# Kernel tuning notes

Measured on AMD Instinct MI355X. Metric: run time of the kernel, lower is better.

Reference implementation:

```python
import jax, jax.numpy as jnp
import numpy as np

HEAD_DIM = 128
N_HEADS = 16
N_KV_HEADS = 4
N_REP = N_HEADS // N_KV_HEADS


def _rope(x, cos, sin):
    # x: [B, S, Hk, D]; cos/sin: [S, D/2]
    xr = x.reshape(*x.shape[:-1], -1, 2)
    x0, x1 = xr[..., 0], xr[..., 1]
    c = cos[None, :, None, :]
    s = sin[None, :, None, :]
    o0 = x0 * c - x1 * s
    o1 = x0 * s + x1 * c
    return jnp.stack([o0, o1], axis=-1).reshape(x.shape)


def setup_inputs() -> dict:
    key = jax.random.key(0)
    ks = jax.random.split(key, 7)
    B, S, DIM = 2, 1024, 2048
    KV_DIM = HEAD_DIM * N_KV_HEADS
    x = jax.random.normal(ks[0], (B, S, DIM), dtype=jnp.float32)
    # rotary angles like LLaMA: freqs = 1/10000^(2i/D)
    inv_freq = 1.0 / (10000.0 ** (np.arange(0, HEAD_DIM, 2, dtype=np.float32) / HEAD_DIM))
    ang = np.arange(S, dtype=np.float32)[:, None] * inv_freq[None, :]  # [S, D/2]
    theta_cos = jnp.asarray(np.cos(ang))
    theta_sin = jnp.asarray(np.sin(ang))
    sc = 0.02
    wq = jax.random.normal(ks[1], (DIM, DIM), dtype=jnp.float32) * sc
    wk = jax.random.normal(ks[2], (DIM, KV_DIM), dtype=jnp.float32) * sc
    wv = jax.random.normal(ks[3], (DIM, KV_DIM), dtype=jnp.float32) * sc
    wo = jax.random.normal(ks[4], (DIM, DIM), dtype=jnp.float32) * sc
    return {"x": x, "theta_cos": theta_cos, "theta_sin": theta_sin,
            "wq": wq, "wk": wk, "wv": wv, "wo": wo}


def reference(x, theta_cos, theta_sin, wq, wk, wv, wo):
    B, S, DIM = x.shape
    # projections
    xq = (x @ wq).reshape(B, S, N_HEADS, HEAD_DIM).transpose(0, 2, 1, 3)  # [B,H,S,D]
    xk = (x @ wk).reshape(B, S, N_KV_HEADS, HEAD_DIM)                      # [B,S,Hk,D]
    xv = (x @ wv).reshape(B, S, N_KV_HEADS, HEAD_DIM)
    # RoPE on K and V only (faithful to source: Q is NOT rotated)
    xk = _rope(xk, theta_cos, theta_sin)
    xv = _rope(xv, theta_cos, theta_sin)
    # GQA repeat: [B,S,Hk,D] -> [B,H,S,D] (each kv head repeated consecutively)
    xk = jnp.repeat(xk.transpose(0, 2, 1, 3), N_REP, axis=1)
    xv = jnp.repeat(xv.transpose(0, 2, 1, 3), N_REP, axis=1)
    scale = HEAD_DIM ** (-0.5)
    att = jnp.einsum('bhqd,bhkd->bhqk', xq, xk) * scale
    # faithful masking: tril then masked_fill(att == 0, -inf)
    tri = jnp.tril(jnp.ones((S, S), dtype=bool))
    att = jnp.where(tri[None, None], att, 0.0)
    att = jnp.where(att == 0.0, -jnp.inf, att)
    att = jax.nn.softmax(att, axis=-1)
    y = jnp.einsum('bhqk,bhkd->bhqd', att, xv)
    out = y.transpose(0, 2, 1, 3).reshape(B, S, DIM)
    return out @ wo
```

## Files before the change

kernel.cpp:

```cpp
#include <hip/hip_runtime.h>
#include <hip/hip_bf16.h>
#include <stdint.h>

typedef _Float16 half_t;
typedef __attribute__((ext_vector_type(2))) _Float16 h2_t;
typedef __attribute__((ext_vector_type(4))) _Float16 h4_t;
typedef __attribute__((ext_vector_type(8))) _Float16 h8_t;
typedef __attribute__((ext_vector_type(4))) float f32x4;

__device__ __forceinline__ void gload16(const void* g, void* l) {
    __builtin_amdgcn_global_load_lds(
        (const __attribute__((address_space(1))) uint32_t*)(uintptr_t)g,
        (__attribute__((address_space(3))) uint32_t*)(uint32_t)(uintptr_t)l,
        16, 0, 0);
}

__global__ __launch_bounds__(256) void prep(const float* __restrict__ x, half_t* __restrict__ xh,
                                            const float* __restrict__ wq, const float* __restrict__ wk,
                                            const float* __restrict__ wv, const float* __restrict__ wo,
                                            half_t* __restrict__ qt, half_t* __restrict__ kt,
                                            half_t* __restrict__ vt, half_t* __restrict__ ot) {
    __shared__ half_t T[32][36];
    const int bx = blockIdx.x;
    if (bx < 2048) {
        int g = (bx * 256 + threadIdx.x) * 8;
        float4 a = *(const float4*)(x + g);
        float4 b = *(const float4*)(x + g + 4);
        h8_t o = {(half_t)a.x,(half_t)a.y,(half_t)a.z,(half_t)a.w,
                  (half_t)b.x,(half_t)b.y,(half_t)b.z,(half_t)b.w};
        *(h8_t*)(xh + g) = o;
        return;
    }
    const int wb = bx - 2048;
    const float* src; half_t* dst; int Nd, t;
    if (wb < 4096)      { src = wq; dst = qt; Nd = 2048; t = wb; }
    else if (wb < 5120) { src = wk; dst = kt; Nd = 512;  t = wb - 4096; }
    else if (wb < 6144) { src = wv; dst = vt; Nd = 512;  t = wb - 5120; }
    else                { src = wo; dst = ot; Nd = 2048; t = wb - 6144; }
    const int K = 2048;
    int nt = Nd >> 5;
    int ti = t / nt, tj = t % nt;
    int r  = threadIdx.x >> 3;
    int c4 = (threadIdx.x & 7) << 2;
    float4 v = *(const float4*)(src + (size_t)(ti*32 + r) * Nd + tj*32 + c4);
    T[r][c4+0] = (half_t)v.x; T[r][c4+1] = (half_t)v.y;
    T[r][c4+2] = (half_t)v.z; T[r][c4+3] = (half_t)v.w;
    __syncthreads();
    h4_t o = {T[c4+0][r], T[c4+1][r], T[c4+2][r], T[c4+3][r]};
    *(h4_t*)(dst + (size_t)(tj*32 + r) * K + ti*32 + c4) = o;
}

template<int BM, int QKV, typename CT>
__global__ __launch_bounds__(256) void gemm_t(const half_t* __restrict__ A,
                                              const half_t* __restrict__ Bq,
                                              const half_t* __restrict__ Bk,
                                              const half_t* __restrict__ Bv,
                                              CT* __restrict__ Cq,
                                              half_t* __restrict__ Ck,
                                              half_t* __restrict__ Cv,
                                              int NB, int K) {
    constexpr int MI  = BM / 32;
    constexpr int ACH = BM / 8;
    constexpr int TOT = ACH + 16;
    constexpr int PW  = TOT / 4;
    __shared__ half_t Ah[BM * 64];
    __shared__ half_t Bh[128 * 64];
    const int tid = threadIdx.x, lane = tid & 63, wid = tid >> 6;
    const int lr = lane & 15, lg = lane >> 4;
    const int wm = wid >> 1, wn = wid & 1;
    const int nwg = gridDim.x, bid = blockIdx.x;
    const int swz = (bid & 7) * (nwg >> 3) + (bid >> 3);
    const int bm = swz / NB, bn = swz % NB;
    const int m0 = bm * BM;

    const half_t* W; CT* Cc; int cs, col0;
    if constexpr (QKV) {
        if (bn < 16)      { W = Bq + (size_t)bn * 128 * K;        Cc = Cq;       cs = 2048; col0 = bn * 128; }
        else if (bn < 20) { W = Bk + (size_t)(bn - 16) * 128 * K; Cc = (CT*)Ck;  cs = 512;  col0 = (bn - 16) * 128; }
        else              { W = Bv + (size_t)(bn - 20) * 128 * K; Cc = (CT*)Cv;  cs = 512;  col0 = (bn - 20) * 128; }
    } else {
        W = Bq + (size_t)bn * 128 * K; Cc = Cq; cs = NB * 128; col0 = bn * 128;
    }

    const half_t* Arow = A + (size_t)m0 * K;
    f32x4 acc[MI][4] = {};

    for (int k0 = 0; k0 < K; k0 += 64) {
        #pragma unroll
        for (int c = 0; c < PW; c++) {
            const int chunk = wid * PW + c;
            const int o = lane * 16;
            if (chunk < ACH) {
                const int go   = (chunk << 10) + o;
                const int row  = go >> 7;
                const int colb = (go & 127) ^ ((row & 7) << 4);
                gload16(Arow + (size_t)row * K + k0 + (colb >> 1), (char*)Ah + (chunk << 10));
            } else {
                const int go   = ((chunk - ACH) << 10) + o;
                const int row  = go >> 7;
                const int colb = (go & 127) ^ ((row & 7) << 4);
                gload16(W + (size_t)row * K + k0 + (colb >> 1), (char*)Bh + ((chunk - ACH) << 10));
            }
        }
        __syncthreads();
        h8_t af[2][MI], bf[2][4];
        #pragma unroll
        for (int kk = 0; kk < 2; kk++) {
            #pragma unroll
            for (int mi = 0; mi < MI; mi++) {
                const int row = wm * (BM / 2) + mi * 16 + lr;
                const int cb  = (kk * 64 + lg * 16) ^ ((lr & 7) << 4);
                af[kk][mi] = *(const h8_t*)((const char*)Ah + row * 128 + cb);
            }
            #pragma unroll
            for (int ni = 0; ni < 4; ni++) {
                const int row = wn * 64 + ni * 16 + lr;
                const int cb  = (kk * 64 + lg * 16) ^ ((lr & 7) << 4);
                bf[kk][ni] = *(const h8_t*)((const char*)Bh + row * 128 + cb);
            }
        }
        #pragma unroll
        for (int kk = 0; kk < 2; kk++)
            #pragma unroll
            for (int mi = 0; mi < MI; mi++)
                #pragma unroll
                for (int ni = 0; ni < 4; ni++)
                    acc[mi][ni] = __builtin_amdgcn_mfma_f32_16x16x32_f16(af[kk][mi], bf[kk][ni], acc[mi][ni], 0, 0, 0);
        __syncthreads();
    }

    #pragma unroll
    for (int mi = 0; mi < MI; mi++)
        #pragma unroll
        for (int ni = 0; ni < 4; ni++)
            #pragma unroll
            for (int r = 0; r < 4; r++) {
                int row = m0 + wm * (BM / 2) + mi * 16 + lg * 4 + r;
                int col = col0 + wn * 64 + ni * 16 + lr;
                Cc[(size_t)row * cs + col] = (CT)acc[mi][ni][r];
            }
}

__global__ __launch_bounds__(256) void rope(half_t* __restrict__ Kh, const half_t* __restrict__ Vh,
                                            half_t* __restrict__ Vt, const float* __restrict__ cs,
                                            const float* __restrict__ sn) {
    const int bx = blockIdx.x;
    if (bx < 2048) {
        int gid = bx * 256 + threadIdx.x;
        int row = gid >> 8;
        int pc  = gid & 255;
        int s   = row & 1023;
        int p   = pc & 63;
        float c = cs[s * 64 + p], si = sn[s * 64 + p];
        h2_t v = *(h2_t*)(Kh + (size_t)row * 512 + 2 * pc);
        float x0 = (float)v[0], x1 = (float)v[1];
        h2_t o = {(half_t)(x0 * c - x1 * si), (half_t)(x0 * si + x1 * c)};
        *(h2_t*)(Kh + (size_t)row * 512 + 2 * pc) = o;
        return;
    }
    int gid = (bx - 2048) * 256 + threadIdx.x;
    int col = gid & 2047;
    int dp  = gid >> 11;
    int s   = col & 1023;
    int p   = dp & 63;
    float c = cs[s * 64 + p], si = sn[s * 64 + p];
    h2_t v = *(const h2_t*)(Vh + (size_t)col * 512 + 2 * dp);
    float x0 = (float)v[0], x1 = (float)v[1];
    Vt[(size_t)(2 * dp)     * 2048 + col] = (half_t)(x0 * c - x1 * si);
    Vt[(size_t)(2 * dp + 1) * 2048 + col] = (half_t)(x0 * si + x1 * c);
}

__global__ __launch_bounds__(256) void attn4(const half_t* __restrict__ Qh, const half_t* __restrict__ Kh,
                                             const half_t* __restrict__ Vtg, half_t* __restrict__ Yh) {
    __shared__ half_t K0[64 * 128], K1[64 * 128];
    __shared__ half_t V0[128 * 64], V1[128 * 64];
    __shared__ half_t Pl[4][16][72];

    const int tid = threadIdx.x, lane = tid & 63, wid = tid >> 6;
    const int lr = lane & 15, lg = lane >> 4;
    const int bx = blockIdx.x;
    const int g  = bx & 7;
    const int local = bx >> 3;
    const int b = g >> 2, kvh = g & 3;
    const int h = kvh * 4 + (local & 3);
    const int li = local >> 2;
    const int qt = (li < 8) ? (15 - li) : (li - 8);
    const int nkb = qt + 1;
    const int qbase = qt * 64 + wid * 16;
    const size_t qrow0 = (size_t)(b * 1024 + qbase);
    const size_t kbase = (size_t)b * 1024;

    const float sc = 0.08838834764831845f;
    h8_t qf[4];
    #pragma unroll
    for (int kk = 0; kk < 4; kk++) {
        qf[kk] = *(const h8_t*)(Qh + (qrow0 + lr) * 2048 + h * 128 + kk * 32 + lg * 8);
        qf[kk] = qf[kk] * (half_t)sc;
    }

    float m[4], l[4];
    f32x4 yacc[8] = {};
    #pragma unroll
    for (int r = 0; r < 4; r++) { m[r] = -1e30f; l[r] = 0.f; }

    auto stage = [&](half_t* kt, half_t* vb, int kb) {
        const int j = kb * 64;
        #pragma unroll
        for (int c = 0; c < 4; c++) {
            const int chunk = wid * 4 + c;
            const int o = (chunk << 10) + lane * 16;
            { const int row  = o >> 8;
              const int colb = (o & 255) ^ ((row & 7) << 4);
              gload16(Kh + (kbase + j + row) * 512 + kvh * 128 + (colb >> 1),
                      (char*)kt + (chunk << 10)); }
            { const int row  = o >> 7;
              const int colb = (o & 127) ^ ((row & 7) << 4);
              gload16(Vtg + (size_t)(kvh * 128 + row) * 2048 + kbase + j + (colb >> 1),
                      (char*)vb + (chunk << 10)); }
        }
    };

    auto iter = [&](const half_t* kt, const half_t* vb, int kb) {
        const int j = kb * 64;
        f32x4 st[4] = {};
        #pragma unroll
        for (int t = 0; t < 4; t++)
            #pragma unroll
            for (int kk = 0; kk < 4; kk++) {
                const int row = t * 16 + lr;
                const int cb  = (kk * 64 + lg * 16) ^ ((lr & 7) << 4);
                h8_t kf = *(const h8_t*)((const char*)kt + row * 256 + cb);
                st[t] = __builtin_amdgcn_mfma_f32_16x16x32_f16(qf[kk], kf, st[t], 0, 0, 0);
            }
        if (kb == nkb - 1) {
            #pragma unroll
            for (int t = 0; t < 4; t++)
                #pragma unroll
                for (int r = 0; r < 4; r++) {
                    int q = qbase + lg * 4 + r;
                    if (j + t * 16 + lr > q) st[t][r] = -1e30f;
                }
        }
        float mb[4];
        #pragma unroll
        for (int r = 0; r < 4; r++)
            mb[r] = fmaxf(fmaxf(st[0][r], st[1][r]), fmaxf(st[2][r], st[3][r]));
        #pragma unroll
        for (int off = 1; off < 16; off <<= 1)
            #pragma unroll
            for (int r = 0; r < 4; r++)
                mb[r] = fmaxf(mb[r], __shfl_xor(mb[r], off));
        float al[4];
        #pragma unroll
        for (int r = 0; r < 4; r++) {
            float mn = fmaxf(m[r], mb[r]);
            al[r] = __expf(m[r] - mn);
            m[r]  = mn;
        }
        float rs[4] = {0.f, 0.f, 0.f, 0.f};
        #pragma unroll
        for (int t = 0; t < 4; t++)
            #pragma unroll
            for (int r = 0; r < 4; r++) {
                float p = __expf(st[t][r] - m[r]);
                st[t][r] = p;
                rs[r] += p;
            }
        #pragma unroll
        for (int off = 1; off < 16; off <<= 1)
            #pragma unroll
            for (int r = 0; r < 4; r++)
                rs[r] += __shfl_xor(rs[r], off);
        #pragma unroll
        for (int r = 0; r < 4; r++) l[r] = l[r] * al[r] + rs[r];
        #pragma unroll
        for (int dt = 0; dt < 8; dt++)
            #pragma unroll
            for (int r = 0; r < 4; r++)
                yacc[dt][r] *= al[r];
        #pragma unroll
        for (int t = 0; t < 4; t++)
            #pragma unroll
            for (int r = 0; r < 4; r++)
                Pl[wid][lg * 4 + r][t * 16 + lr] = (half_t)st[t][r];
        h8_t pa0 = *(const h8_t*)(&Pl[wid][lr][lg * 8]);
        h8_t pa1 = *(const h8_t*)(&Pl[wid][lr][32 + lg * 8]);
        #pragma unroll
        for (int dt = 0; dt < 8; dt++) {
            const int row = dt * 16 + lr;
            const int cb0 = (lg * 16) ^ ((lr & 7) << 4);
            const int cb1 = (64 + lg * 16) ^ ((lr & 7) << 4);
            h8_t v0 = *(const h8_t*)((const char*)vb + row * 128 + cb0);
            h8_t v1 = *(const h8_t*)((const char*)vb + row * 128 + cb1);
            yacc[dt] = __builtin_amdgcn_mfma_f32_16x16x32_f16(pa0, v0, yacc[dt], 0, 0, 0);
            yacc[dt] = __builtin_amdgcn_mfma_f32_16x16x32_f16(pa1, v1, yacc[dt], 0, 0, 0);
        }
    };

    stage(K0, V0, 0);
    __syncthreads();
    for (int kb = 0; kb < nkb; kb += 2) {
        if (kb + 1 < nkb) stage(K1, V1, kb + 1);
        iter(K0, V0, kb);
        __syncthreads();
        if (kb + 1 < nkb) {
            if (kb + 2 < nkb) stage(K0, V0, kb + 2);
            iter(K1, V1, kb + 1);
            __syncthreads();
        }
    }

    #pragma unroll
    for (int r = 0; r < 4; r++) l[r] = 1.0f / l[r];
    #pragma unroll
    for (int dt = 0; dt < 8; dt++)
        #pragma unroll
        for (int r = 0; r < 4; r++)
            Yh[(qrow0 + lg * 4 + r) * 2048 + h * 128 + dt * 16 + lr] = (half_t)(yacc[dt][r] * l[r]);
}

extern "C" void kernel_launch(void* const* d_in, const int* in_sizes, int n_in,
                              void* d_out, int out_size, void* d_ws, size_t ws_size,
                              hipStream_t stream) {
    const float* x  = (const float*)d_in[0];
    const float* tc = (const float*)d_in[1];
    const float* ts = (const float*)d_in[2];
    const float* wq = (const float*)d_in[3];
    const float* wk = (const float*)d_in[4];
    const float* wv = (const float*)d_in[5];
    const float* wo = (const float*)d_in[6];
    float* out = (float*)d_out;

    const size_t MD = 2048ull * 2048, MK = 2048ull * 512;
    half_t* Xh  = (half_t*)d_ws;
    half_t* Qh  = Xh  + MD;
    half_t* Kh  = Qh  + MD;
    half_t* Vh  = Kh  + MK;
    half_t* Vt  = Vh  + MK;
    half_t* Yh  = Vt  + MK;
    half_t* wqt = Yh  + MD;
    half_t* wkt = wqt + MD;
    half_t* wvt = wkt + MK;
    half_t* wot = wvt + MK;

    prep<<<12288, 256, 0, stream>>>(x, Xh, wq, wk, wv, wo, wqt, wkt, wvt, wot);
    gemm_t<64, 1, half_t><<<768, 256, 0, stream>>>(Xh, wqt, wkt, wvt, Qh, Kh, Vh, 24, 2048);
    rope<<<4096, 256, 0, stream>>>(Kh, Vh, Vt, tc, ts);
    attn4<<<512, 256, 0, stream>>>(Qh, Kh, Vt, Yh);
    gemm_t<64, 0, float><<<512, 256, 0, stream>>>(Yh, wot, nullptr, nullptr, out, nullptr, nullptr, 16, 2048);
}
```

Baseline: 122.5 us.

## Pair low and high causal query tiles per attention block to share K/V loads

Each attention block now handles two query tiles, t and 15-t, so every block does the same amount of causal work. The K/V tiles staged in shared memory are reused by both query tiles for the first t+1 key blocks. Grid size halves from 512 to 256 blocks. In exchange, register pressure roughly doubles (two accumulator sets and two sets of softmax state), which may cut occupancy, and 256 blocks may not fill all CUs well.

```diff
diff --git a/kernel.cpp b/kernel.cpp
--- a/kernel.cpp
+++ b/kernel.cpp
@@ -170,11 +170,11 @@
     Vt[(size_t)(2 * dp + 1) * 2048 + col] = (half_t)(x0 * si + x1 * c);
 }
 
-__global__ __launch_bounds__(256) void attn4(const half_t* __restrict__ Qh, const half_t* __restrict__ Kh,
+__global__ __launch_bounds__(256) void attn5(const half_t* __restrict__ Qh, const half_t* __restrict__ Kh,
                                              const half_t* __restrict__ Vtg, half_t* __restrict__ Yh) {
     __shared__ half_t K0[64 * 128], K1[64 * 128];
     __shared__ half_t V0[128 * 64], V1[128 * 64];
-    __shared__ half_t Pl[4][16][72];
+    __shared__ half_t Pl[4][2][16][72];
 
     const int tid = threadIdx.x, lane = tid & 63, wid = tid >> 6;
     const int lr = lane & 15, lg = lane >> 4;
@@ -183,25 +183,29 @@
     const int local = bx >> 3;
     const int b = g >> 2, kvh = g & 3;
     const int h = kvh * 4 + (local & 3);
-    const int li = local >> 2;
-    const int qt = (li < 8) ? (15 - li) : (li - 8);
-    const int nkb = qt + 1;
-    const int qbase = qt * 64 + wid * 16;
-    const size_t qrow0 = (size_t)(b * 1024 + qbase);
+    const int t = local >> 2;
+    const int qtl = t, qth = 15 - t;
+    const int nkb = qth + 1;
+    const int qbl = qtl * 64 + wid * 16;
+    const int qbh = qth * 64 + wid * 16;
+    const size_t qrl = (size_t)(b * 1024 + qbl);
+    const size_t qrh = (size_t)(b * 1024 + qbh);
     const size_t kbase = (size_t)b * 1024;
 
     const float sc = 0.08838834764831845f;
-    h8_t qf[4];
+    h8_t qf[2][4];
     #pragma unroll
     for (int kk = 0; kk < 4; kk++) {
-        qf[kk] = *(const h8_t*)(Qh + (qrow0 + lr) * 2048 + h * 128 + kk * 32 + lg * 8);
-        qf[kk] = qf[kk] * (half_t)sc;
-    }
-
-    float m[4], l[4];
-    f32x4 yacc[8] = {};
+        qf[0][kk] = *(const h8_t*)(Qh + (qrl + lr) * 2048 + h * 128 + kk * 32 + lg * 8) * (half_t)sc;
+        qf[1][kk] = *(const h8_t*)(Qh + (qrh + lr) * 2048 + h * 128 + kk * 32 + lg * 8) * (half_t)sc;
+    }
+
+    float m[2][4], l[2][4];
+    f32x4 yacc[2][8] = {};
     #pragma unroll
-    for (int r = 0; r < 4; r++) { m[r] = -1e30f; l[r] = 0.f; }
+    for (int u = 0; u < 2; u++)
+        #pragma unroll
+        for (int r = 0; r < 4; r++) { m[u][r] = -1e30f; l[u][r] = 0.f; }
 
     auto stage = [&](half_t* kt, half_t* vb, int kb) {
         const int j = kb * 64;
@@ -222,69 +226,79 @@
 
     auto iter = [&](const half_t* kt, const half_t* vb, int kb) {
         const int j = kb * 64;
-        f32x4 st[4] = {};
-        #pragma unroll
-        for (int t = 0; t < 4; t++)
+        const bool a0 = (kb <= qtl);
+        f32x4 st[2][4] = {};
+        #pragma unroll
+        for (int t4 = 0; t4 < 4; t4++)
             #pragma unroll
             for (int kk = 0; kk < 4; kk++) {
-                const int row = t * 16 + lr;
+                const int row = t4 * 16 + lr;
                 const int cb  = (kk * 64 + lg * 16) ^ ((lr & 7) << 4);
                 h8_t kf = *(const h8_t*)((const char*)kt + row * 256 + cb);
-                st[t] = __builtin_amdgcn_mfma_f32_16x16x32_f16(qf[kk], kf, st[t], 0, 0, 0);
-            }
-        if (kb == nkb - 1) {
-            #pragma unroll
-            for (int t = 0; t < 4; t++)
+                st[1][t4] = __builtin_amdgcn_mfma_f32_16x16x32_f16(qf[1][kk], kf, st[1][t4], 0, 0, 0);
+                if (a0)
+                    st[0][t4] = __builtin_amdgcn_mfma_f32_16x16x32_f16(qf[0][kk], kf, st[0][t4], 0, 0, 0);
+            }
+        h8_t pa[2][2];
+        #pragma unroll
+        for (int u = 0; u < 2; u++) {
+            if (u == 0 && !a0) continue;
+            const int qb   = u ? qbh : qbl;
+            const bool dia = (kb == (u ? qth : qtl));
+            if (dia) {
+                #pragma unroll
+                for (int t4 = 0; t4 < 4; t4++)
+                    #pragma unroll
+                    for (int r = 0; r < 4; r++) {
+                        int q = qb + lg * 4 + r;
+                        if (j + t4 * 16 + lr > q) st[u][t4][r] = -1e30f;
+                    }
+            }
+            float mb[4];
+            #pragma unroll
+            for (int r = 0; r < 4; r++)
+                mb[r] = fmaxf(fmaxf(st[u][0][r], st[u][1][r]), fmaxf(st[u][2][r], st[u][3][r]));
+            #pragma unroll
+            for (int off = 1; off < 16; off <<= 1)
+                #pragma unroll
+                for (int r = 0; r < 4; r++)
+                    mb[r] = fmaxf(mb[r], __shfl_xor(mb[r], off));
+            float al[4];
+            #pragma unroll
+            for (int r = 0; r < 4; r++) {
+                float mn = fmaxf(m[u][r], mb[r]);
+                al[r]   = __expf(m[u][r] - mn);
+                m[u][r] = mn;
+            }
+            float rs[4] = {0.f, 0.f, 0.f, 0.f};
+            #pragma unroll
+            for (int t4 = 0; t4 < 4; t4++)
                 #pragma unroll
                 for (int r = 0; r < 4; r++) {
-                    int q = qbase + lg * 4 + r;
-                    if (j + t * 16 + lr > q) st[t][r] = -1e30f;
+                    float p = __expf(st[u][t4][r] - m[u][r]);
+                    st[u][t4][r] = p;
+                    rs[r] += p;
                 }
-        }
-        float mb[4];
-        #pragma unroll
-        for (int r = 0; r < 4; r++)
-            mb[r] = fmaxf(fmaxf(st[0][r], st[1][r]), fmaxf(st[2][r], st[3][r]));
-        #pragma unroll
-        for (int off = 1; off < 16; off <<= 1)
-            #pragma unroll
-            for (int r = 0; r < 4; r++)
-                mb[r] = fmaxf(mb[r], __shfl_xor(mb[r], off));
-        float al[4];
-        #pragma unroll
-        for (int r = 0; r < 4; r++) {
-            float mn = fmaxf(m[r], mb[r]);
-            al[r] = __expf(m[r] - mn);
-            m[r]  = mn;
-        }
-        float rs[4] = {0.f, 0.f, 0.f, 0.f};
-        #pragma unroll
-        for (int t = 0; t < 4; t++)
-            #pragma unroll
-            for (int r = 0; r < 4; r++) {
-                float p = __expf(st[t][r] - m[r]);
-                st[t][r] = p;
-                rs[r] += p;
-            }
-        #pragma unroll
-        for (int off = 1; off < 16; off <<= 1)
-            #pragma unroll
-            for (int r = 0; r < 4; r++)
-                rs[r] += __shfl_xor(rs[r], off);
-        #pragma unroll
-        for (int r = 0; r < 4; r++) l[r] = l[r] * al[r] + rs[r];
-        #pragma unroll
-        for (int dt = 0; dt < 8; dt++)
-            #pragma unroll
-            for (int r = 0; r < 4; r++)
-                yacc[dt][r] *= al[r];
-        #pragma unroll
-        for (int t = 0; t < 4; t++)
-            #pragma unroll
-            for (int r = 0; r < 4; r++)
-                Pl[wid][lg * 4 + r][t * 16 + lr] = (half_t)st[t][r];
-        h8_t pa0 = *(const h8_t*)(&Pl[wid][lr][lg * 8]);
-        h8_t pa1 = *(const h8_t*)(&Pl[wid][lr][32 + lg * 8]);
+            #pragma unroll
+            for (int off = 1; off < 16; off <<= 1)
+                #pragma unroll
+                for (int r = 0; r < 4; r++)
+                    rs[r] += __shfl_xor(rs[r], off);
+            #pragma unroll
+            for (int r = 0; r < 4; r++) l[u][r] = l[u][r] * al[r] + rs[r];
+            #pragma unroll
+            for (int dt = 0; dt < 8; dt++)
+                #pragma unroll
+                for (int r = 0; r < 4; r++)
+                    yacc[u][dt][r] *= al[r];
+            #pragma unroll
+            for (int t4 = 0; t4 < 4; t4++)
+                #pragma unroll
+                for (int r = 0; r < 4; r++)
+                    Pl[wid][u][lg * 4 + r][t4 * 16 + lr] = (half_t)st[u][t4][r];
+            pa[u][0] = *(const h8_t*)(&Pl[wid][u][lr][lg * 8]);
+            pa[u][1] = *(const h8_t*)(&Pl[wid][u][lr][32 + lg * 8]);
+        }
         #pragma unroll
         for (int dt = 0; dt < 8; dt++) {
             const int row = dt * 16 + lr;
@@ -292,8 +306,12 @@
             const int cb1 = (64 + lg * 16) ^ ((lr & 7) << 4);
             h8_t v0 = *(const h8_t*)((const char*)vb + row * 128 + cb0);
             h8_t v1 = *(const h8_t*)((const char*)vb + row * 128 + cb1);
-            yacc[dt] = __builtin_amdgcn_mfma_f32_16x16x32_f16(pa0, v0, yacc[dt], 0, 0, 0);
-            yacc[dt] = __builtin_amdgcn_mfma_f32_16x16x32_f16(pa1, v1, yacc[dt], 0, 0, 0);
+            yacc[1][dt] = __builtin_amdgcn_mfma_f32_16x16x32_f16(pa[1][0], v0, yacc[1][dt], 0, 0, 0);
+            yacc[1][dt] = __builtin_amdgcn_mfma_f32_16x16x32_f16(pa[1][1], v1, yacc[1][dt], 0, 0, 0);
+            if (a0) {
+                yacc[0][dt] = __builtin_amdgcn_mfma_f32_16x16x32_f16(pa[0][0], v0, yacc[0][dt], 0, 0, 0);
+                yacc[0][dt] = __builtin_amdgcn_mfma_f32_16x16x32_f16(pa[0][1], v1, yacc[0][dt], 0, 0, 0);
+            }
         }
     };
 
@@ -311,12 +329,16 @@
     }
 
     #pragma unroll
-    for (int r = 0; r < 4; r++) l[r] = 1.0f / l[r];
-    #pragma unroll
-    for (int dt = 0; dt < 8; dt++)
-        #pragma unroll
-        for (int r = 0; r < 4; r++)
-            Yh[(qrow0 + lg * 4 + r) * 2048 + h * 128 + dt * 16 + lr] = (half_t)(yacc[dt][r] * l[r]);
+    for (int u = 0; u < 2; u++) {
+        const size_t qr = u ? qrh : qrl;
+        #pragma unroll
+        for (int r = 0; r < 4; r++) {
+            float inv = 1.0f / l[u][r];
+            #pragma unroll
+            for (int dt = 0; dt < 8; dt++)
+                Yh[(qr + lg * 4 + r) * 2048 + h * 128 + dt * 16 + lr] = (half_t)(yacc[u][dt][r] * inv);
+        }
+    }
 }
 
 extern "C" void kernel_launch(void* const* d_in, const int* in_sizes, int n_in,
@@ -346,6 +368,6 @@
     prep<<<12288, 256, 0, stream>>>(x, Xh, wq, wk, wv, wo, wqt, wkt, wvt, wot);
     gemm_t<64, 1, half_t><<<768, 256, 0, stream>>>(Xh, wqt, wkt, wvt, Qh, Kh, Vh, 24, 2048);
     rope<<<4096, 256, 0, stream>>>(Kh, Vh, Vt, tc, ts);
-    attn4<<<512, 256, 0, stream>>>(Qh, Kh, Vt, Yh);
+    attn5<<<256, 256, 0, stream>>>(Qh, Kh, Vt, Yh);
     gemm_t<64, 0, float><<<512, 256, 0, stream>>>(Yh, wot, nullptr, nullptr, out, nullptr, nullptr, 16, 2048);
 }
```

After: 132.9 us. 8.5% more time.
